# Performance work log

Measured on AMD Instinct MI355X. Metric: run time of the kernel, lower is better.

## Reference

```python
import jax, jax.numpy as jnp
import numpy as np

DIM = 7168
N_EXPERTS = 256
TOPK = 8            # n_activated_experts
N_GROUPS = 8        # n_expert_groups
TOPK_GROUPS = 4     # n_limited_groups
ROUTE_SCALE = 2.5
N_TOKENS = 8192


def setup_inputs() -> dict:
    key = jax.random.key(0)
    k1, k2, k3 = jax.random.split(key, 3)
    x = jax.random.normal(k1, (N_TOKENS, DIM), dtype=jnp.float32)
    weight = jax.random.normal(k2, (N_EXPERTS, DIM), dtype=jnp.float32) * 0.02
    bias = jax.random.normal(k3, (N_EXPERTS,), dtype=jnp.float32) * 0.01
    return {"x": x, "weight": weight, "bias": bias}


def reference(x, weight, bias):
    B = x.shape[0]
    # router scores: [B, n_experts]
    logits = jnp.einsum('bd,ed->be', x, weight)
    scores = jax.nn.softmax(logits, axis=-1)
    original_scores = scores
    # bias is active because dim == 7168
    s = (scores + bias).reshape(B, N_GROUPS, N_EXPERTS // N_GROUPS)
    # with bias: group score = sum of top-2 expert scores in the group
    group_scores = jax.lax.top_k(s, 2)[0].sum(axis=-1)          # [B, G]
    gidx = jax.lax.top_k(group_scores, TOPK_GROUPS)[1]          # [B, topk_groups]
    # keep mask: True for selected groups (inverse of torch's scatter-False mask)
    keep = jnp.zeros((B, N_GROUPS), dtype=bool).at[
        jnp.arange(B)[:, None], gidx].set(True)
    s = jnp.where(keep[:, :, None], s, -jnp.inf).reshape(B, N_EXPERTS)
    indices = jax.lax.top_k(s, TOPK)[1]                          # [B, topk]
    weights = jnp.take_along_axis(original_scores, indices, axis=1) * ROUTE_SCALE
    return weights, indices
```

## Files before the change

### kernel.cpp

```cpp
#include <hip/hip_runtime.h>
#include <cstddef>
#include <cstdint>

#define DIM   7168
#define NEXP  256
#define NTOK  8192
#define BM    64
#define BK    32

typedef _Float16 f16;
typedef __attribute__((ext_vector_type(8))) _Float16 f16x8;
typedef __attribute__((ext_vector_type(4))) float    f32x4;

__global__ __launch_bounds__(256) void wconv(const float* __restrict__ W,
                                             f16* __restrict__ Whi,
                                             f16* __restrict__ Wlo) {
  const int i = (blockIdx.x * 256 + threadIdx.x) * 4;
  const float4 v = *reinterpret_cast<const float4*>(W + i);
  f16 h0 = (f16)v.x, h1 = (f16)v.y, h2 = (f16)v.z, h3 = (f16)v.w;
  f16 l0 = (f16)(v.x - (float)h0), l1 = (f16)(v.y - (float)h1);
  f16 l2 = (f16)(v.z - (float)h2), l3 = (f16)(v.w - (float)h3);
  __attribute__((ext_vector_type(4))) _Float16 hv = {h0, h1, h2, h3};
  __attribute__((ext_vector_type(4))) _Float16 lv = {l0, l1, l2, l3};
  *reinterpret_cast<decltype(hv)*>(Whi + i) = hv;
  *reinterpret_cast<decltype(lv)*>(Wlo + i) = lv;
}

__global__ __launch_bounds__(256, 2) void gemm_mfma(const float* __restrict__ X,
                                                    const f16* __restrict__ Whi,
                                                    const f16* __restrict__ Wlo,
                                                    float* __restrict__ L,
                                                    int ktiles) {
  __shared__ __align__(16) f16 Ahi[BM * BK];
  __shared__ __align__(16) f16 Alo[BM * BK];
  __shared__ __align__(16) f16 Bhi[NEXP * BK];
  __shared__ __align__(16) f16 Blo[NEXP * BK];

  const int tid  = threadIdx.x;
  const int lane = tid & 63;
  const int w    = tid >> 6;
  const int bm   = blockIdx.x * BM;
  const int kbase = blockIdx.y * ktiles * BK;
  float* Lp = L + (size_t)blockIdx.y * NTOK * NEXP;

  const int ar  = tid >> 2;
  const int akq = tid & 3;
  const float* asrc = X + (size_t)(bm + ar) * DIM + akq * 8;

  const int aoff = (lane & 15) * BK + (lane >> 4) * 8;
  const int boff = (w * 64 + (lane & 15)) * BK + (lane >> 4) * 8;

  f32x4 acc[4][4];
#pragma unroll
  for (int i = 0; i < 4; ++i)
#pragma unroll
    for (int j = 0; j < 4; ++j) acc[i][j] = 0.0f;

  for (int t = 0; t < ktiles; ++t) {
    const int k0 = kbase + t * BK;

    __syncthreads();

#pragma unroll
    for (int j = 0; j < 4; ++j) {
      const int u0 = w * 256 + j * 64;
      const int u  = u0 + lane;
      const size_t goff = (size_t)(u >> 2) * DIM + k0 + (u & 3) * 8;
      __builtin_amdgcn_global_load_lds(
          (const __attribute__((address_space(1))) void*)(Whi + goff),
          (__attribute__((address_space(3))) void*)(&Bhi[u0 * 8]), 16, 0, 0);
      __builtin_amdgcn_global_load_lds(
          (const __attribute__((address_space(1))) void*)(Wlo + goff),
          (__attribute__((address_space(3))) void*)(&Blo[u0 * 8]), 16, 0, 0);
    }

    const float4 a0 = *reinterpret_cast<const float4*>(asrc + k0);
    const float4 a1 = *reinterpret_cast<const float4*>(asrc + k0 + 4);
    const float av[8] = {a0.x, a0.y, a0.z, a0.w, a1.x, a1.y, a1.z, a1.w};
    f16x8 hv, lv;
#pragma unroll
    for (int j = 0; j < 8; ++j) {
      const f16 h = (f16)av[j];
      hv[j] = h;
      lv[j] = (f16)(av[j] - (float)h);
    }
    *reinterpret_cast<f16x8*>(&Ahi[tid * 8]) = hv;
    *reinterpret_cast<f16x8*>(&Alo[tid * 8]) = lv;

    __syncthreads();

    f16x8 ah[4], al[4];
#pragma unroll
    for (int mi = 0; mi < 4; ++mi) {
      ah[mi] = *reinterpret_cast<const f16x8*>(&Ahi[mi * 512 + aoff]);
      al[mi] = *reinterpret_cast<const f16x8*>(&Alo[mi * 512 + aoff]);
    }
#pragma unroll
    for (int ni = 0; ni < 4; ++ni) {
      const f16x8 bh = *reinterpret_cast<const f16x8*>(&Bhi[ni * 512 + boff]);
      const f16x8 bl = *reinterpret_cast<const f16x8*>(&Blo[ni * 512 + boff]);
#pragma unroll
      for (int mi = 0; mi < 4; ++mi) {
        acc[mi][ni] = __builtin_amdgcn_mfma_f32_16x16x32_f16(ah[mi], bh, acc[mi][ni], 0, 0, 0);
        acc[mi][ni] = __builtin_amdgcn_mfma_f32_16x16x32_f16(al[mi], bh, acc[mi][ni], 0, 0, 0);
        acc[mi][ni] = __builtin_amdgcn_mfma_f32_16x16x32_f16(ah[mi], bl, acc[mi][ni], 0, 0, 0);
      }
    }
  }

  const int orow0 = bm + (lane >> 4) * 4;
  const int ocol  = w * 64 + (lane & 15);
#pragma unroll
  for (int mi = 0; mi < 4; ++mi)
#pragma unroll
    for (int j = 0; j < 4; ++j) {
      const int row = orow0 + mi * 16 + j;
#pragma unroll
      for (int ni = 0; ni < 4; ++ni)
        Lp[(size_t)row * NEXP + ocol + ni * 16] = acc[mi][ni][j];
    }
}

__global__ __launch_bounds__(256) void routing(const float* __restrict__ L,
                                               const float* __restrict__ bias,
                                               float* __restrict__ out,
                                               int nparts) {
  const int lane = threadIdx.x & 63;
  const int tok  = (int)((blockIdx.x * blockDim.x + threadIdx.x) >> 6);
  if (tok >= NTOK) return;

  float4 v = {0.f, 0.f, 0.f, 0.f};
  for (int p = 0; p < nparts; ++p) {
    const float4 t = reinterpret_cast<const float4*>(
        L + (size_t)p * NTOK * NEXP + (size_t)tok * NEXP)[lane];
    v.x += t.x; v.y += t.y; v.z += t.z; v.w += t.w;
  }

  float m = fmaxf(fmaxf(v.x, v.y), fmaxf(v.z, v.w));
#pragma unroll
  for (int off = 32; off; off >>= 1) m = fmaxf(m, __shfl_xor(m, off));
  float s0 = expf(v.x - m), s1 = expf(v.y - m), s2 = expf(v.z - m), s3 = expf(v.w - m);
  float sum = s0 + s1 + s2 + s3;
#pragma unroll
  for (int off = 32; off; off >>= 1) sum += __shfl_xor(sum, off);
  const float inv = 1.0f / sum;
  s0 *= inv; s1 *= inv; s2 *= inv; s3 *= inv;

  const float4 bb = reinterpret_cast<const float4*>(bias)[lane];
  float b0 = s0 + bb.x, b1 = s1 + bb.y, b2 = s2 + bb.z, b3 = s3 + bb.w;

  float m1 = fmaxf(b0, b1), m2 = fminf(b0, b1);
  if (b2 > m1) { m2 = m1; m1 = b2; } else m2 = fmaxf(m2, b2);
  if (b3 > m1) { m2 = m1; m1 = b3; } else m2 = fmaxf(m2, b3);
#pragma unroll
  for (int off = 1; off < 8; off <<= 1) {
    const float o1 = __shfl_xor(m1, off);
    const float o2 = __shfl_xor(m2, off);
    if (o1 > m1) { m2 = fmaxf(m1, o2); m1 = o1; } else m2 = fmaxf(m2, o1);
  }
  const float gscore = m1 + m2;

  float gs[8];
#pragma unroll
  for (int g = 0; g < 8; ++g) gs[g] = __shfl(gscore, g * 8);

  unsigned gsel = 0;
#pragma unroll
  for (int k = 0; k < 4; ++k) {
    float best = -INFINITY; int bi = 0;
#pragma unroll
    for (int g = 0; g < 8; ++g)
      if (!((gsel >> g) & 1u) && gs[g] > best) { best = gs[g]; bi = g; }
    gsel |= 1u << bi;
  }
  if (!((gsel >> (lane >> 3)) & 1u)) { b0 = b1 = b2 = b3 = -INFINITY; }

  float outw = 0.0f, outi = 0.0f;
  for (int k = 0; k < 8; ++k) {
    float bv = b0; int bi = 0;
    if (b1 > bv) { bv = b1; bi = 1; }
    if (b2 > bv) { bv = b2; bi = 2; }
    if (b3 > bv) { bv = b3; bi = 3; }
    float rv = bv; int ri = lane * 4 + bi;
#pragma unroll
    for (int off = 32; off; off >>= 1) {
      const float ov = __shfl_xor(rv, off);
      const int   oi = __shfl_xor(ri, off);
      if (ov > rv || (ov == rv && oi < ri)) { rv = ov; ri = oi; }
    }
    const int srcl = ri >> 2, slot = ri & 3;
    const float sv = (slot == 0) ? s0 : (slot == 1) ? s1 : (slot == 2) ? s2 : s3;
    const float wsel = __shfl(sv, srcl) * 2.5f;
    if (lane == k) { outw = wsel; outi = (float)ri; }
    if (lane == srcl) {
      if      (slot == 0) b0 = -INFINITY;
      else if (slot == 1) b1 = -INFINITY;
      else if (slot == 2) b2 = -INFINITY;
      else                b3 = -INFINITY;
    }
  }
  if (lane < 8) {
    out[(size_t)tok * 8 + lane] = outw;
    out[(size_t)NTOK * 8 + (size_t)tok * 8 + lane] = outi;
  }
}

extern "C" void kernel_launch(void* const* d_in, const int* in_sizes, int n_in,
                              void* d_out, int out_size, void* d_ws, size_t ws_size,
                              hipStream_t stream) {
  const float* x    = (const float*)d_in[0];
  const float* w    = (const float*)d_in[1];
  const float* bias = (const float*)d_in[2];
  float* out = (float*)d_out;

  const size_t part_bytes = (size_t)NTOK * NEXP * sizeof(float);
  const size_t w_bytes    = (size_t)NEXP * DIM * sizeof(f16);
  int nparts = 1;
  for (int np = 8; np >= 1; np >>= 1)
    if ((size_t)np * part_bytes + 2 * w_bytes <= ws_size) { nparts = np; break; }

  float* logits = (float*)d_ws;
  f16* whi = (f16*)((char*)d_ws + (size_t)nparts * part_bytes);
  f16* wlo = whi + (size_t)NEXP * DIM;

  wconv<<<(NEXP * DIM) / (256 * 4), 256, 0, stream>>>(w, whi, wlo);

  const int ktiles = (DIM / BK) / nparts;
  dim3 gridG(NTOK / BM, nparts);
  gemm_mfma<<<gridG, 256, 0, stream>>>(x, whi, wlo, logits, ktiles);

  routing<<<NTOK / 4, 256, 0, stream>>>(logits, bias, out, nparts);
}
```

Measured before the change: 416.5 us.

## Double-buffer LDS tiles in split-f16 MFMA router GEMM

```diff
diff --git a/kernel.cpp b/kernel.cpp
--- a/kernel.cpp
+++ b/kernel.cpp
@@ -31,10 +31,10 @@
                                                     const f16* __restrict__ Wlo,
                                                     float* __restrict__ L,
                                                     int ktiles) {
-  __shared__ __align__(16) f16 Ahi[BM * BK];
-  __shared__ __align__(16) f16 Alo[BM * BK];
-  __shared__ __align__(16) f16 Bhi[NEXP * BK];
-  __shared__ __align__(16) f16 Blo[NEXP * BK];
+  __shared__ __align__(16) f16 Ah[2][BM * BK];
+  __shared__ __align__(16) f16 Al[2][BM * BK];
+  __shared__ __align__(16) f16 Bh[2][NEXP * BK];
+  __shared__ __align__(16) f16 Bl[2][NEXP * BK];
 
   const int tid  = threadIdx.x;
   const int lane = tid & 63;
@@ -56,11 +56,13 @@
 #pragma unroll
     for (int j = 0; j < 4; ++j) acc[i][j] = 0.0f;
 
-  for (int t = 0; t < ktiles; ++t) {
-    const int k0 = kbase + t * BK;
-
-    __syncthreads();
-
+  float4 pa0, pa1;
+
+  auto aload = [&](int k0) {
+    pa0 = *reinterpret_cast<const float4*>(asrc + k0);
+    pa1 = *reinterpret_cast<const float4*>(asrc + k0 + 4);
+  };
+  auto stageB = [&](int buf, int k0) {
 #pragma unroll
     for (int j = 0; j < 4; ++j) {
       const int u0 = w * 256 + j * 64;
@@ -68,15 +70,14 @@
       const size_t goff = (size_t)(u >> 2) * DIM + k0 + (u & 3) * 8;
       __builtin_amdgcn_global_load_lds(
           (const __attribute__((address_space(1))) void*)(Whi + goff),
-          (__attribute__((address_space(3))) void*)(&Bhi[u0 * 8]), 16, 0, 0);
+          (__attribute__((address_space(3))) void*)(&Bh[buf][u0 * 8]), 16, 0, 0);
       __builtin_amdgcn_global_load_lds(
           (const __attribute__((address_space(1))) void*)(Wlo + goff),
-          (__attribute__((address_space(3))) void*)(&Blo[u0 * 8]), 16, 0, 0);
-    }
-
-    const float4 a0 = *reinterpret_cast<const float4*>(asrc + k0);
-    const float4 a1 = *reinterpret_cast<const float4*>(asrc + k0 + 4);
-    const float av[8] = {a0.x, a0.y, a0.z, a0.w, a1.x, a1.y, a1.z, a1.w};
+          (__attribute__((address_space(3))) void*)(&Bl[buf][u0 * 8]), 16, 0, 0);
+    }
+  };
+  auto awrite = [&](int buf) {
+    const float av[8] = {pa0.x, pa0.y, pa0.z, pa0.w, pa1.x, pa1.y, pa1.z, pa1.w};
     f16x8 hv, lv;
 #pragma unroll
     for (int j = 0; j < 8; ++j) {
@@ -84,28 +85,46 @@
       hv[j] = h;
       lv[j] = (f16)(av[j] - (float)h);
     }
-    *reinterpret_cast<f16x8*>(&Ahi[tid * 8]) = hv;
-    *reinterpret_cast<f16x8*>(&Alo[tid * 8]) = lv;
-
+    *reinterpret_cast<f16x8*>(&Ah[buf][tid * 8]) = hv;
+    *reinterpret_cast<f16x8*>(&Al[buf][tid * 8]) = lv;
+  };
+  auto compute = [&](int buf) {
+    f16x8 ah[4], al4[4];
+#pragma unroll
+    for (int mi = 0; mi < 4; ++mi) {
+      ah[mi]  = *reinterpret_cast<const f16x8*>(&Ah[buf][mi * 512 + aoff]);
+      al4[mi] = *reinterpret_cast<const f16x8*>(&Al[buf][mi * 512 + aoff]);
+    }
+#pragma unroll
+    for (int ni = 0; ni < 4; ++ni) {
+      const f16x8 bh = *reinterpret_cast<const f16x8*>(&Bh[buf][ni * 512 + boff]);
+      const f16x8 bl = *reinterpret_cast<const f16x8*>(&Bl[buf][ni * 512 + boff]);
+#pragma unroll
+      for (int mi = 0; mi < 4; ++mi) {
+        acc[mi][ni] = __builtin_amdgcn_mfma_f32_16x16x32_f16(ah[mi],  bh, acc[mi][ni], 0, 0, 0);
+        acc[mi][ni] = __builtin_amdgcn_mfma_f32_16x16x32_f16(al4[mi], bh, acc[mi][ni], 0, 0, 0);
+        acc[mi][ni] = __builtin_amdgcn_mfma_f32_16x16x32_f16(ah[mi],  bl, acc[mi][ni], 0, 0, 0);
+      }
+    }
+  };
+
+  aload(kbase);
+  stageB(0, kbase);
+  awrite(0);
+  __syncthreads();
+
+  int cur = 0;
+  for (int t = 0; t < ktiles; ++t) {
+    const int nxt = cur ^ 1;
+    if (t + 1 < ktiles) {
+      const int k1 = kbase + (t + 1) * BK;
+      aload(k1);
+      stageB(nxt, k1);
+      awrite(nxt);
+    }
+    compute(cur);
     __syncthreads();
-
-    f16x8 ah[4], al[4];
-#pragma unroll
-    for (int mi = 0; mi < 4; ++mi) {
-      ah[mi] = *reinterpret_cast<const f16x8*>(&Ahi[mi * 512 + aoff]);
-      al[mi] = *reinterpret_cast<const f16x8*>(&Alo[mi * 512 + aoff]);
-    }
-#pragma unroll
-    for (int ni = 0; ni < 4; ++ni) {
-      const f16x8 bh = *reinterpret_cast<const f16x8*>(&Bhi[ni * 512 + boff]);
-      const f16x8 bl = *reinterpret_cast<const f16x8*>(&Blo[ni * 512 + boff]);
-#pragma unroll
-      for (int mi = 0; mi < 4; ++mi) {
-        acc[mi][ni] = __builtin_amdgcn_mfma_f32_16x16x32_f16(ah[mi], bh, acc[mi][ni], 0, 0, 0);
-        acc[mi][ni] = __builtin_amdgcn_mfma_f32_16x16x32_f16(al[mi], bh, acc[mi][ni], 0, 0, 0);
-        acc[mi][ni] = __builtin_amdgcn_mfma_f32_16x16x32_f16(ah[mi], bl, acc[mi][ni], 0, 0, 0);
-      }
-    }
+    cur = nxt;
   }
 
   const int orow0 = bm + (lane >> 4) * 4;
```

New measurement: 422.2 us. Within noise of the previous version (+1.4%).

## Double GEMM M-tile to 128 rows and widen split-K candidate set

Applied to the files above, without the earlier changes.

```diff
diff --git a/kernel.cpp b/kernel.cpp
--- a/kernel.cpp
+++ b/kernel.cpp
@@ -5,7 +5,7 @@
 #define DIM   7168
 #define NEXP  256
 #define NTOK  8192
-#define BM    64
+#define BM    128
 #define BK    32
 
 typedef _Float16 f16;
@@ -31,10 +31,10 @@
                                                     const f16* __restrict__ Wlo,
                                                     float* __restrict__ L,
                                                     int ktiles) {
-  __shared__ __align__(16) f16 Ahi[BM * BK];
-  __shared__ __align__(16) f16 Alo[BM * BK];
-  __shared__ __align__(16) f16 Bhi[NEXP * BK];
-  __shared__ __align__(16) f16 Blo[NEXP * BK];
+  __shared__ __align__(16) f16 Ah[BM * BK];
+  __shared__ __align__(16) f16 Al[BM * BK];
+  __shared__ __align__(16) f16 Bh[NEXP * BK];
+  __shared__ __align__(16) f16 Bl[NEXP * BK];
 
   const int tid  = threadIdx.x;
   const int lane = tid & 63;
@@ -43,21 +43,26 @@
   const int kbase = blockIdx.y * ktiles * BK;
   float* Lp = L + (size_t)blockIdx.y * NTOK * NEXP;
 
-  const int ar  = tid >> 2;
-  const int akq = tid & 3;
-  const float* asrc = X + (size_t)(bm + ar) * DIM + akq * 8;
+  const int ar = tid >> 1;
+  const int ah_ = tid & 1;
+  const float* asrc = X + (size_t)(bm + ar) * DIM + ah_ * 16;
 
   const int aoff = (lane & 15) * BK + (lane >> 4) * 8;
   const int boff = (w * 64 + (lane & 15)) * BK + (lane >> 4) * 8;
 
-  f32x4 acc[4][4];
-#pragma unroll
-  for (int i = 0; i < 4; ++i)
+  f32x4 acc[8][4];
+#pragma unroll
+  for (int i = 0; i < 8; ++i)
 #pragma unroll
     for (int j = 0; j < 4; ++j) acc[i][j] = 0.0f;
 
   for (int t = 0; t < ktiles; ++t) {
     const int k0 = kbase + t * BK;
+
+    const float4 v0 = *reinterpret_cast<const float4*>(asrc + k0);
+    const float4 v1 = *reinterpret_cast<const float4*>(asrc + k0 + 4);
+    const float4 v2 = *reinterpret_cast<const float4*>(asrc + k0 + 8);
+    const float4 v3 = *reinterpret_cast<const float4*>(asrc + k0 + 12);
 
     __syncthreads();
 
@@ -68,42 +73,50 @@
       const size_t goff = (size_t)(u >> 2) * DIM + k0 + (u & 3) * 8;
       __builtin_amdgcn_global_load_lds(
           (const __attribute__((address_space(1))) void*)(Whi + goff),
-          (__attribute__((address_space(3))) void*)(&Bhi[u0 * 8]), 16, 0, 0);
+          (__attribute__((address_space(3))) void*)(&Bh[u0 * 8]), 16, 0, 0);
       __builtin_amdgcn_global_load_lds(
           (const __attribute__((address_space(1))) void*)(Wlo + goff),
-          (__attribute__((address_space(3))) void*)(&Blo[u0 * 8]), 16, 0, 0);
-    }
-
-    const float4 a0 = *reinterpret_cast<const float4*>(asrc + k0);
-    const float4 a1 = *reinterpret_cast<const float4*>(asrc + k0 + 4);
-    const float av[8] = {a0.x, a0.y, a0.z, a0.w, a1.x, a1.y, a1.z, a1.w};
-    f16x8 hv, lv;
-#pragma unroll
-    for (int j = 0; j < 8; ++j) {
-      const f16 h = (f16)av[j];
-      hv[j] = h;
-      lv[j] = (f16)(av[j] - (float)h);
-    }
-    *reinterpret_cast<f16x8*>(&Ahi[tid * 8]) = hv;
-    *reinterpret_cast<f16x8*>(&Alo[tid * 8]) = lv;
+          (__attribute__((address_space(3))) void*)(&Bl[u0 * 8]), 16, 0, 0);
+    }
+
+    {
+      const float av[16] = {v0.x, v0.y, v0.z, v0.w, v1.x, v1.y, v1.z, v1.w,
+                            v2.x, v2.y, v2.z, v2.w, v3.x, v3.y, v3.z, v3.w};
+      f16x8 hA, lA, hB, lB;
+#pragma unroll
+      for (int j = 0; j < 8; ++j) {
+        const f16 h = (f16)av[j];
+        hA[j] = h; lA[j] = (f16)(av[j] - (float)h);
+      }
+#pragma unroll
+      for (int j = 0; j < 8; ++j) {
+        const f16 h = (f16)av[8 + j];
+        hB[j] = h; lB[j] = (f16)(av[8 + j] - (float)h);
+      }
+      const int abase = ar * BK + ah_ * 16;
+      *reinterpret_cast<f16x8*>(&Ah[abase])     = hA;
+      *reinterpret_cast<f16x8*>(&Ah[abase + 8]) = hB;
+      *reinterpret_cast<f16x8*>(&Al[abase])     = lA;
+      *reinterpret_cast<f16x8*>(&Al[abase + 8]) = lB;
+    }
 
     __syncthreads();
 
-    f16x8 ah[4], al[4];
-#pragma unroll
-    for (int mi = 0; mi < 4; ++mi) {
-      ah[mi] = *reinterpret_cast<const f16x8*>(&Ahi[mi * 512 + aoff]);
-      al[mi] = *reinterpret_cast<const f16x8*>(&Alo[mi * 512 + aoff]);
-    }
+    f16x8 bh[4], bl[4];
 #pragma unroll
     for (int ni = 0; ni < 4; ++ni) {
-      const f16x8 bh = *reinterpret_cast<const f16x8*>(&Bhi[ni * 512 + boff]);
-      const f16x8 bl = *reinterpret_cast<const f16x8*>(&Blo[ni * 512 + boff]);
-#pragma unroll
-      for (int mi = 0; mi < 4; ++mi) {
-        acc[mi][ni] = __builtin_amdgcn_mfma_f32_16x16x32_f16(ah[mi], bh, acc[mi][ni], 0, 0, 0);
-        acc[mi][ni] = __builtin_amdgcn_mfma_f32_16x16x32_f16(al[mi], bh, acc[mi][ni], 0, 0, 0);
-        acc[mi][ni] = __builtin_amdgcn_mfma_f32_16x16x32_f16(ah[mi], bl, acc[mi][ni], 0, 0, 0);
+      bh[ni] = *reinterpret_cast<const f16x8*>(&Bh[ni * 512 + boff]);
+      bl[ni] = *reinterpret_cast<const f16x8*>(&Bl[ni * 512 + boff]);
+    }
+#pragma unroll
+    for (int mi = 0; mi < 8; ++mi) {
+      const f16x8 a_h = *reinterpret_cast<const f16x8*>(&Ah[mi * 512 + aoff]);
+      const f16x8 a_l = *reinterpret_cast<const f16x8*>(&Al[mi * 512 + aoff]);
+#pragma unroll
+      for (int ni = 0; ni < 4; ++ni) {
+        acc[mi][ni] = __builtin_amdgcn_mfma_f32_16x16x32_f16(a_h, bh[ni], acc[mi][ni], 0, 0, 0);
+        acc[mi][ni] = __builtin_amdgcn_mfma_f32_16x16x32_f16(a_l, bh[ni], acc[mi][ni], 0, 0, 0);
+        acc[mi][ni] = __builtin_amdgcn_mfma_f32_16x16x32_f16(a_h, bl[ni], acc[mi][ni], 0, 0, 0);
       }
     }
   }
@@ -111,7 +124,7 @@
   const int orow0 = bm + (lane >> 4) * 4;
   const int ocol  = w * 64 + (lane & 15);
 #pragma unroll
-  for (int mi = 0; mi < 4; ++mi)
+  for (int mi = 0; mi < 8; ++mi)
 #pragma unroll
     for (int j = 0; j < 4; ++j) {
       const int row = orow0 + mi * 16 + j;
@@ -215,9 +228,10 @@
 
   const size_t part_bytes = (size_t)NTOK * NEXP * sizeof(float);
   const size_t w_bytes    = (size_t)NEXP * DIM * sizeof(f16);
+  const int cand[7] = {16, 14, 8, 7, 4, 2, 1};
   int nparts = 1;
-  for (int np = 8; np >= 1; np >>= 1)
-    if ((size_t)np * part_bytes + 2 * w_bytes <= ws_size) { nparts = np; break; }
+  for (int c = 0; c < 7; ++c)
+    if ((size_t)cand[c] * part_bytes + 2 * w_bytes <= ws_size) { nparts = cand[c]; break; }
 
   float* logits = (float*)d_ws;
   f16* whi = (f16*)((char*)d_ws + (size_t)nparts * part_bytes);
```

Result: faster. 404.4 us (-2.9%).
